# Optimization experiments

Measured on AMD Instinct MI355X. Metric: run time of the kernel, lower is better.

## Reference

```python
import jax, jax.numpy as jnp
import numpy as np

B, T, I, H, O = 64, 512, 128, 1024, 128
ALPHA = 0.2


def setup_inputs() -> dict:
    key = jax.random.key(0)
    ks = jax.random.split(key, 7)
    inv_sqrt_h = 1.0 / np.sqrt(H)
    return {
        "x": jax.random.normal(ks[0], (B, T, I), dtype=jnp.float32),
        "wi": jax.random.normal(ks[1], (I, H), dtype=jnp.float32) / np.sqrt(I),
        "wrec": jax.random.normal(ks[2], (H, H), dtype=jnp.float32) * inv_sqrt_h,
        "wout": jax.random.normal(ks[3], (H, O), dtype=jnp.float32) * inv_sqrt_h,
        "b": jax.random.normal(ks[4], (H, 1), dtype=jnp.float32) * 0.1,
        "g": jax.random.normal(ks[5], (H, 1), dtype=jnp.float32) * 0.5 + 1.0,
        "h0": jax.random.normal(ks[6], (H,), dtype=jnp.float32) * 0.1,
    }


def reference(x, wi, wrec, wout, b, g, h0):
    # Leaky tanh RNN: h_{t+1} = h_t + alpha*(-h_t + (g*r_t) @ wrec^T + x_t @ wi)
    #                 r_t = tanh(h_t + b); out_t = (g*r_t) @ wout
    gv = g[:, 0]  # (H,)
    bv = b[:, 0]  # (H,)
    batch = x.shape[0]

    r0 = jnp.tanh(h0 + bv)                     # (H,)
    out0 = (gv * r0) @ wout                    # (O,) broadcast over batch

    h_init = jnp.broadcast_to(h0, (batch, h0.shape[0]))
    r_init = jnp.broadcast_to(r0, (batch, h0.shape[0]))

    # precompute input projection for all steps used in the loop (steps 0..T-2)
    xs = jnp.swapaxes(x[:, :-1, :], 0, 1)      # (T-1, B, I)

    def step(carry, x_t):
        h, r = carry
        h = h + ALPHA * (-h + (gv * r) @ wrec.T + x_t @ wi)
        r = jnp.tanh(h + bv)
        out = (gv * r) @ wout                  # (B, O)
        return (h, r), out

    _, outs = jax.lax.scan(step, (h_init, r_init), xs)   # (T-1, B, O)
    outs = jnp.swapaxes(outs, 0, 1)                      # (B, T-1, O)
    out0b = jnp.broadcast_to(out0, (batch, 1, wout.shape[1]))
    return jnp.concatenate([out0b, outs], axis=1)        # (B, T, O)
```

## Files before the change

kernel.cpp:

```cpp
#include <hip/hip_runtime.h>

#define H 1024
#define I_DIM 128
#define O_DIM 128
#define T_DIM 512
#define ALPHA 0.2f
#define NWG 64
#define GSZ 16
#define SLICE_U64 96
#define GRP_U64   (64 * SLICE_U64)

typedef short short8 __attribute__((ext_vector_type(8)));
typedef float f32x4 __attribute__((ext_vector_type(4)));
typedef unsigned long long ull_alias __attribute__((may_alias));

__device__ __forceinline__ unsigned short f2b(float f) {
    union { float f; unsigned u; } x; x.f = f;
    unsigned u = x.u;
    return (unsigned short)((u + 0x7FFFu + ((u >> 16) & 1u)) >> 16);
}
__device__ __forceinline__ float tanh_fast(float x) {
    float e = __expf(2.0f * x);
    return 1.0f - 2.0f * __builtin_amdgcn_rcpf(e + 1.0f);
}
__device__ __forceinline__ short8 ld8f(const float* __restrict__ p) {
    const float4 a = *(const float4*)p;
    const float4 b = *(const float4*)(p + 4);
    short8 r;
    r[0]=(short)f2b(a.x); r[1]=(short)f2b(a.y); r[2]=(short)f2b(a.z); r[3]=(short)f2b(a.w);
    r[4]=(short)f2b(b.x); r[5]=(short)f2b(b.y); r[6]=(short)f2b(b.z); r[7]=(short)f2b(b.w);
    return r;
}

__global__ __launch_bounds__(256, 1) void rnn_kernel(
    const float* __restrict__ x, const float* __restrict__ wi,
    const float* __restrict__ wrec, const float* __restrict__ wout,
    const float* __restrict__ bb, const float* __restrict__ gg,
    const float* __restrict__ h0p, float* __restrict__ out,
    unsigned long long* __restrict__ aG)
{
    __shared__ unsigned short abuf[32 * 512];
    __shared__ unsigned short aloc[1024];
    __shared__ float opart[4 * 128];

    const int tid  = threadIdx.x;
    const int w    = tid >> 6, lane = tid & 63;
    const int n    = lane & 15, q = lane >> 4;
    const int grp  = blockIdx.x & 3;
    const int ji   = blockIdx.x >> 2;
    const int j0   = ji * 64;
    const int j    = j0 + w * 16 + n;
    const int b0   = grp * 16;

    short8 wfr[32];
#pragma unroll
    for (int kt = 0; kt < 32; ++kt)
        wfr[kt] = ld8f(&wrec[(size_t)j * H + kt * 32 + q * 8]);

    short8 wifr[4];
#pragma unroll
    for (int kt = 0; kt < 4; ++kt) {
        short8 v;
#pragma unroll
        for (int i = 0; i < 8; ++i)
            v[i] = (short)f2b(wi[(size_t)(kt * 32 + q * 8 + i) * H + j]);
        wifr[kt] = v;
    }
    short8 wofr[8];
#pragma unroll
    for (int kk = 0; kk < 8; ++kk) {
        short8 v;
        const int kb = (w * 8 + kk) * 32 + q * 8;
#pragma unroll
        for (int i = 0; i < 8; ++i)
            v[i] = (n < 8) ? (short)f2b(wout[(size_t)(kb + i) * O_DIM + ji * 8 + n]) : (short)0;
        wofr[kk] = v;
    }

    const float gv = gg[j], bv = bb[j], h00 = h0p[j];
    float hreg[4];
#pragma unroll
    for (int r = 0; r < 4; ++r) hreg[r] = h00;

    const int kl    = w * 16 + n;
    const int off_l = (kl >> 5) * 512 + ((kl & 31) >> 3) * 128 + (kl & 7);
    const int slot  = ji * 4 + w;

    const int c1 = lane,      os1 = c1 / 3, p1 = c1 - os1 * 3;
    const int c2 = lane + 64, os2 = c2 / 3, p2 = c2 - os2 * 3;
    unsigned long long* const pub0 = aG + grp * GRP_U64 + slot * SLICE_U64;
    unsigned long long* const pub1 = pub0 + 4 * GRP_U64;
    const unsigned long long* const con0 = aG + grp * GRP_U64;
    const unsigned long long* const con1 = con0 + 4 * GRP_U64;

    int coff[8];
#pragma unroll
    for (int i = 0; i < 8; ++i) {
        const int kt  = w * 8 + i;
        const int sub = lane >> 4;
        const int pw  = (kt & 1) * 2 + (sub >> 1);
        const int so  = sub & 1;
        const int m   = lane & 15;
        coff[i] = ((kt >> 1) * 4 + pw) * SLICE_U64 + (m * 2 + so) * 3;
    }

    auto pack_chunk = [&](int os, int p) -> unsigned long long {
        const ull_alias* op = (const ull_alias*)&aloc[w * 256 + (os & 1) * 128 + (os >> 1) * 8];
        const unsigned long long lo = op[0], hi = op[1];
        unsigned long long d;
        if (p == 0)      d = lo & 0x0000FFFFFFFFFFFFull;
        else if (p == 1) d = ((lo >> 48) | (hi << 16)) & 0x0000FFFFFFFFFFFFull;
        else             d = ((hi >> 32) | ((hi >> 48) << 32)) & 0x0000FFFFFFFFFFFFull;
        return d;
    };

    auto publish = [&](int t) {
        asm volatile("" ::: "memory");
        const unsigned long long tagv = (unsigned long long)(unsigned)t << 48;
        unsigned long long* dst = (t & 1) ? pub1 : pub0;
        __hip_atomic_store(&dst[c1], pack_chunk(os1, p1) | tagv,
                           __ATOMIC_RELAXED, __HIP_MEMORY_SCOPE_AGENT);
        if (lane < 32)
            __hip_atomic_store(&dst[c2], pack_chunk(os2, p2) | tagv,
                               __ATOMIC_RELAXED, __HIP_MEMORY_SCOPE_AGENT);
    };

    auto consume = [&](int tv) {
        const unsigned tt = (unsigned)tv;
        const unsigned long long* gb = (tv & 1) ? con1 : con0;
        unsigned long long v[24];
        for (;;) {
#pragma unroll
            for (int i = 0; i < 8; ++i) {
                const unsigned long long* cp = gb + coff[i];
                v[3*i  ] = __hip_atomic_load(cp,     __ATOMIC_RELAXED, __HIP_MEMORY_SCOPE_AGENT);
                v[3*i+1] = __hip_atomic_load(cp + 1, __ATOMIC_RELAXED, __HIP_MEMORY_SCOPE_AGENT);
                v[3*i+2] = __hip_atomic_load(cp + 2, __ATOMIC_RELAXED, __HIP_MEMORY_SCOPE_AGENT);
            }
            unsigned bad = 0;
#pragma unroll
            for (int c = 0; c < 24; ++c) bad |= (unsigned)(v[c] >> 48) ^ tt;
            if (__all(bad == 0)) break;
            __builtin_amdgcn_s_sleep(1);
        }
        asm volatile("" ::: "memory");
#pragma unroll
        for (int i = 0; i < 8; ++i) {
            const unsigned long long ca = v[3*i], cb = v[3*i+1], cc = v[3*i+2];
            const unsigned long long w01 = (ca & 0xFFFFFFFFull)
                | (((ca >> 32) & 0xFFFFull) << 32) | ((cb & 0xFFFFull) << 48);
            const unsigned long long w23 = ((cb >> 16) & 0xFFFFFFFFull) | (cc << 32);
            ull_alias* d = (ull_alias*)((char*)abuf + w * 8192 + (i * 64 + lane) * 16);
            d[0] = w01; d[1] = w23;
        }
    };

    auto do_out = [&](int t) {
        f32x4 oa = {0.f, 0.f, 0.f, 0.f};
#pragma unroll
        for (int kk = 0; kk < 8; ++kk) {
            short8 af = *(const short8*)&abuf[(w * 8 + kk) * 512 + lane * 8];
            oa = __builtin_amdgcn_mfma_f32_16x16x32_bf16(af, wofr[kk], oa, 0, 0, 0);
        }
        if (n < 8) {
#pragma unroll
            for (int r = 0; r < 4; ++r) opart[w * 128 + (4 * q + r) * 8 + n] = oa[r];
        }
        __syncthreads();
        if (tid < 128) {
            float s = opart[tid] + opart[128 + tid] + opart[256 + tid] + opart[384 + tid];
            const int m = tid >> 3, c = tid & 7;
            out[((size_t)(b0 + m) * T_DIM + t) * O_DIM + ji * 8 + c] = s;
        }
    };

    {
        unsigned short a0 = f2b(gv * tanh_fast(h00 + bv));
#pragma unroll
        for (int r = 0; r < 4; ++r) aloc[off_l + (4 * q + r) * 8] = a0;
        publish(0);
    }

    short8 xfr[4];
#pragma unroll
    for (int kt = 0; kt < 4; ++kt)
        xfr[kt] = ld8f(&x[(size_t)(b0 + n) * T_DIM * I_DIM + kt * 32 + q * 8]);

    for (int t = 1; t < T_DIM; ++t) {
        f32x4 acc0 = {0.f,0.f,0.f,0.f}, acc1 = {0.f,0.f,0.f,0.f};
        acc0 = __builtin_amdgcn_mfma_f32_16x16x32_bf16(xfr[0], wifr[0], acc0, 0,0,0);
        acc1 = __builtin_amdgcn_mfma_f32_16x16x32_bf16(xfr[1], wifr[1], acc1, 0,0,0);
        acc0 = __builtin_amdgcn_mfma_f32_16x16x32_bf16(xfr[2], wifr[2], acc0, 0,0,0);
        acc1 = __builtin_amdgcn_mfma_f32_16x16x32_bf16(xfr[3], wifr[3], acc1, 0,0,0);

        __syncthreads();
        consume(t - 1);
        __syncthreads();

#pragma unroll
        for (int kt = 0; kt < 32; kt += 2) {
            short8 a0f = *(const short8*)&abuf[kt * 512 + lane * 8];
            short8 a1f = *(const short8*)&abuf[(kt + 1) * 512 + lane * 8];
            acc0 = __builtin_amdgcn_mfma_f32_16x16x32_bf16(a0f, wfr[kt],     acc0, 0,0,0);
            acc1 = __builtin_amdgcn_mfma_f32_16x16x32_bf16(a1f, wfr[kt + 1], acc1, 0,0,0);
        }

#pragma unroll
        for (int r = 0; r < 4; ++r) {
            float z  = acc0[r] + acc1[r];
            float hv = (1.0f - ALPHA) * hreg[r] + ALPHA * z;
            hreg[r] = hv;
            aloc[off_l + (4 * q + r) * 8] = f2b(gv * tanh_fast(hv + bv));
        }
        publish(t);

        if (t < T_DIM - 1) {
#pragma unroll
            for (int kt = 0; kt < 4; ++kt)
                xfr[kt] = ld8f(&x[((size_t)(b0 + n) * T_DIM + t) * I_DIM + kt * 32 + q * 8]);
        }
        do_out(t - 1);
    }

    __syncthreads();
    consume(T_DIM - 1);
    __syncthreads();
    do_out(T_DIM - 1);
}

extern "C" void kernel_launch(void* const* d_in, const int* in_sizes, int n_in,
                              void* d_out, int out_size, void* d_ws, size_t ws_size,
                              hipStream_t stream) {
    const float* x    = (const float*)d_in[0];
    const float* wi   = (const float*)d_in[1];
    const float* wrec = (const float*)d_in[2];
    const float* wout = (const float*)d_in[3];
    const float* bb   = (const float*)d_in[4];
    const float* gg   = (const float*)d_in[5];
    const float* h0   = (const float*)d_in[6];
    float* outp = (float*)d_out;

    unsigned long long* aG = (unsigned long long*)d_ws;

    hipMemsetAsync(d_ws, 0xFF, (size_t)2 * 4 * GRP_U64 * 8, stream);
    hipLaunchKernelGGL(rnn_kernel, dim3(NWG), dim3(256), 0, stream,
                       x, wi, wrec, wout, bb, gg, h0, outp, aG);
}
```

Before: 2.122 ms.

## Reorganize cross-workgroup activation exchange into planar layout and prefetch x earlier

Changes the global exchange buffer from per-slot 96-u64 slices to three planes of 2048 u64s. Each lane's publish and consume accesses become contiguous and coalesced across the wavefront, and consumers scatter the unpacked chunks into abuf through precomputed offsets. The next step's x row is now loaded as raw float4 at the top of the loop and converted to bf16 later, so its global load latency overlaps the recurrent wait and matmul. This costs extra registers for the prefetched floats and a more complex index mapping that has to match the producer packing exactly.

```diff
diff --git a/kernel.cpp b/kernel.cpp
--- a/kernel.cpp
+++ b/kernel.cpp
@@ -7,8 +7,8 @@
 #define ALPHA 0.2f
 #define NWG 64
 #define GSZ 16
-#define SLICE_U64 96
-#define GRP_U64   (64 * SLICE_U64)
+#define PLANE_U64 2048
+#define GRP_U64   (3 * PLANE_U64)
 
 typedef short short8 __attribute__((ext_vector_type(8)));
 typedef float f32x4 __attribute__((ext_vector_type(4)));
@@ -26,6 +26,12 @@
 __device__ __forceinline__ short8 ld8f(const float* __restrict__ p) {
     const float4 a = *(const float4*)p;
     const float4 b = *(const float4*)(p + 4);
+    short8 r;
+    r[0]=(short)f2b(a.x); r[1]=(short)f2b(a.y); r[2]=(short)f2b(a.z); r[3]=(short)f2b(a.w);
+    r[4]=(short)f2b(b.x); r[5]=(short)f2b(b.y); r[6]=(short)f2b(b.z); r[7]=(short)f2b(b.w);
+    return r;
+}
+__device__ __forceinline__ short8 pack8(float4 a, float4 b) {
     short8 r;
     r[0]=(short)f2b(a.x); r[1]=(short)f2b(a.y); r[2]=(short)f2b(a.z); r[3]=(short)f2b(a.w);
     r[4]=(short)f2b(b.x); r[5]=(short)f2b(b.y); r[6]=(short)f2b(b.z); r[7]=(short)f2b(b.w);
@@ -84,73 +90,78 @@
 
     const int kl    = w * 16 + n;
     const int off_l = (kl >> 5) * 512 + ((kl & 31) >> 3) * 128 + (kl & 7);
-    const int slot  = ji * 4 + w;
-
-    const int c1 = lane,      os1 = c1 / 3, p1 = c1 - os1 * 3;
-    const int c2 = lane + 64, os2 = c2 / 3, p2 = c2 - os2 * 3;
-    unsigned long long* const pub0 = aG + grp * GRP_U64 + slot * SLICE_U64;
-    unsigned long long* const pub1 = pub0 + 4 * GRP_U64;
-    const unsigned long long* const con0 = aG + grp * GRP_U64;
-    const unsigned long long* const con1 = con0 + 4 * GRP_U64;
-
-    int coff[8];
+    const int s_sl  = ji * 4 + w;
+
+    unsigned long long* const gB0 = aG + grp * GRP_U64;
+    unsigned long long* const gB1 = aG + (4 + grp) * GRP_U64;
+
+    const int pubA = (lane >> 5) * PLANE_U64 + s_sl * 32 + (lane & 31);
+    const int pubB = 2 * PLANE_U64 + s_sl * 32 + lane;
+    const int oA   = lane & 31;
+
+    const int cbase = w * 512 + lane;
+
+    int doff[8];
 #pragma unroll
     for (int i = 0; i < 8; ++i) {
-        const int kt  = w * 8 + i;
-        const int sub = lane >> 4;
-        const int pw  = (kt & 1) * 2 + (sub >> 1);
-        const int so  = sub & 1;
-        const int m   = lane & 15;
-        coff[i] = ((kt >> 1) * 4 + pw) * SLICE_U64 + (m * 2 + so) * 3;
-    }
-
-    auto pack_chunk = [&](int os, int p) -> unsigned long long {
-        const ull_alias* op = (const ull_alias*)&aloc[w * 256 + (os & 1) * 128 + (os >> 1) * 8];
-        const unsigned long long lo = op[0], hi = op[1];
-        unsigned long long d;
-        if (p == 0)      d = lo & 0x0000FFFFFFFFFFFFull;
-        else if (p == 1) d = ((lo >> 48) | (hi << 16)) & 0x0000FFFFFFFFFFFFull;
-        else             d = ((hi >> 32) | ((hi >> 48) << 32)) & 0x0000FFFFFFFFFFFFull;
-        return d;
-    };
+        const int idx = i * 64 + lane;
+        const int s   = 16 * w + (idx >> 5);
+        const int oo  = idx & 31;
+        const int m   = oo >> 1, so = oo & 1;
+        const int k0  = (s >> 2) * 64 + (s & 3) * 16 + so * 8;
+        doff[i] = ((k0 >> 5) * 512 + ((k0 & 31) >> 3) * 128 + m * 8) * 2;
+    }
 
     auto publish = [&](int t) {
         asm volatile("" ::: "memory");
         const unsigned long long tagv = (unsigned long long)(unsigned)t << 48;
-        unsigned long long* dst = (t & 1) ? pub1 : pub0;
-        __hip_atomic_store(&dst[c1], pack_chunk(os1, p1) | tagv,
-                           __ATOMIC_RELAXED, __HIP_MEMORY_SCOPE_AGENT);
-        if (lane < 32)
-            __hip_atomic_store(&dst[c2], pack_chunk(os2, p2) | tagv,
+        unsigned long long* gb = (t & 1) ? gB1 : gB0;
+        {
+            const ull_alias* opq = (const ull_alias*)&aloc[w * 256 + (oA & 1) * 128 + (oA >> 1) * 8];
+            const unsigned long long lo = opq[0], hi = opq[1];
+            const unsigned long long d0 = lo & 0x0000FFFFFFFFFFFFull;
+            const unsigned long long d1 = ((lo >> 48) | (hi << 16)) & 0x0000FFFFFFFFFFFFull;
+            __hip_atomic_store(gb + pubA, ((lane < 32) ? d0 : d1) | tagv,
                                __ATOMIC_RELAXED, __HIP_MEMORY_SCOPE_AGENT);
+        }
+        if (lane < 32) {
+            const ull_alias* opq = (const ull_alias*)&aloc[w * 256 + (lane & 1) * 128 + (lane >> 1) * 8];
+            const unsigned long long hi = opq[1];
+            const unsigned long long d2 = ((hi >> 32) & 0xFFFFFFFFull) | tagv;
+            __hip_atomic_store(gb + pubB, d2, __ATOMIC_RELAXED, __HIP_MEMORY_SCOPE_AGENT);
+        }
     };
 
     auto consume = [&](int tv) {
         const unsigned tt = (unsigned)tv;
-        const unsigned long long* gb = (tv & 1) ? con1 : con0;
-        unsigned long long v[24];
+        const unsigned long long* gb = (tv & 1) ? gB1 : gB0;
+        unsigned long long v0[8], v1[8], v2[8];
         for (;;) {
 #pragma unroll
             for (int i = 0; i < 8; ++i) {
-                const unsigned long long* cp = gb + coff[i];
-                v[3*i  ] = __hip_atomic_load(cp,     __ATOMIC_RELAXED, __HIP_MEMORY_SCOPE_AGENT);
-                v[3*i+1] = __hip_atomic_load(cp + 1, __ATOMIC_RELAXED, __HIP_MEMORY_SCOPE_AGENT);
-                v[3*i+2] = __hip_atomic_load(cp + 2, __ATOMIC_RELAXED, __HIP_MEMORY_SCOPE_AGENT);
+                v0[i] = __hip_atomic_load(gb + cbase + i * 64,
+                                          __ATOMIC_RELAXED, __HIP_MEMORY_SCOPE_AGENT);
+                v1[i] = __hip_atomic_load(gb + PLANE_U64 + cbase + i * 64,
+                                          __ATOMIC_RELAXED, __HIP_MEMORY_SCOPE_AGENT);
+                v2[i] = __hip_atomic_load(gb + 2 * PLANE_U64 + cbase + i * 64,
+                                          __ATOMIC_RELAXED, __HIP_MEMORY_SCOPE_AGENT);
             }
             unsigned bad = 0;
 #pragma unroll
-            for (int c = 0; c < 24; ++c) bad |= (unsigned)(v[c] >> 48) ^ tt;
+            for (int i = 0; i < 8; ++i)
+                bad |= ((unsigned)(v0[i] >> 48) ^ tt) | ((unsigned)(v1[i] >> 48) ^ tt)
+                     | ((unsigned)(v2[i] >> 48) ^ tt);
             if (__all(bad == 0)) break;
             __builtin_amdgcn_s_sleep(1);
         }
         asm volatile("" ::: "memory");
 #pragma unroll
         for (int i = 0; i < 8; ++i) {
-            const unsigned long long ca = v[3*i], cb = v[3*i+1], cc = v[3*i+2];
+            const unsigned long long ca = v0[i], cb = v1[i], cc = v2[i];
             const unsigned long long w01 = (ca & 0xFFFFFFFFull)
                 | (((ca >> 32) & 0xFFFFull) << 32) | ((cb & 0xFFFFull) << 48);
             const unsigned long long w23 = ((cb >> 16) & 0xFFFFFFFFull) | (cc << 32);
-            ull_alias* d = (ull_alias*)((char*)abuf + w * 8192 + (i * 64 + lane) * 16);
+            ull_alias* d = (ull_alias*)((char*)abuf + doff[i]);
             d[0] = w01; d[1] = w23;
         }
     };
@@ -186,7 +197,18 @@
     for (int kt = 0; kt < 4; ++kt)
         xfr[kt] = ld8f(&x[(size_t)(b0 + n) * T_DIM * I_DIM + kt * 32 + q * 8]);
 
+    float4 xr[8];
+
     for (int t = 1; t < T_DIM; ++t) {
+        if (t < T_DIM - 1) {
+            const float* xp = &x[((size_t)(b0 + n) * T_DIM + t) * I_DIM];
+#pragma unroll
+            for (int kt = 0; kt < 4; ++kt) {
+                xr[2 * kt]     = *(const float4*)(xp + kt * 32 + q * 8);
+                xr[2 * kt + 1] = *(const float4*)(xp + kt * 32 + q * 8 + 4);
+            }
+        }
+
         f32x4 acc0 = {0.f,0.f,0.f,0.f}, acc1 = {0.f,0.f,0.f,0.f};
         acc0 = __builtin_amdgcn_mfma_f32_16x16x32_bf16(xfr[0], wifr[0], acc0, 0,0,0);
         acc1 = __builtin_amdgcn_mfma_f32_16x16x32_bf16(xfr[1], wifr[1], acc1, 0,0,0);
@@ -217,7 +239,7 @@
         if (t < T_DIM - 1) {
 #pragma unroll
             for (int kt = 0; kt < 4; ++kt)
-                xfr[kt] = ld8f(&x[((size_t)(b0 + n) * T_DIM + t) * I_DIM + kt * 32 + q * 8]);
+                xfr[kt] = pack8(xr[2 * kt], xr[2 * kt + 1]);
         }
         do_out(t - 1);
     }
```

Result: faster. 1.847 ms (-12.9%).
